# Kernel tuning notes

Hardware: AMD Instinct MI355X
Metric: run time of the kernel (lower is better)

Reference implementation:

```python
import jax, jax.numpy as jnp
import numpy as np
import math

B, N, E = 32, 512, 8192          # graphs, nodes/graph, edges/graph
IN_DIM, D, H, HD, L, C = 64, 128, 4, 32, 3, 10
HID = 2 * D                      # _FeatureMLP hidden = max(d, 2*d)


def _ln(x, g, b, eps=1e-5):
    mu = x.mean(-1, keepdims=True)
    var = ((x - mu) ** 2).mean(-1, keepdims=True)
    return (x - mu) / jnp.sqrt(var + eps) * g + b


def _gelu(x):
    return jax.nn.gelu(x, approximate=False)  # torch nn.GELU default (erf)


def setup_inputs() -> dict:
    key = jax.random.key(0)
    ks = iter(jax.random.split(key, 48))
    def w(*shape):
        return jax.random.normal(next(ks), shape, jnp.float32) * 0.02
    z = lambda *s: jnp.zeros(s, jnp.float32)
    o = lambda *s: jnp.ones(s, jnp.float32)
    return {
        'x': jax.random.normal(next(ks), (B * N, IN_DIM), jnp.float32),
        'src': jax.random.randint(next(ks), (B, E), 0, N),
        'dst': jax.random.randint(next(ks), (B, E), 0, N),
        # node encoder: Linear -> LN -> GELU -> Linear -> LN
        'enc_w1': w(IN_DIM, HID), 'enc_b1': z(HID), 'enc_g1': o(HID), 'enc_bn1': z(HID),
        'enc_w2': w(HID, D), 'enc_b2': z(D), 'enc_g2': o(D), 'enc_bn2': z(D),
        # per-layer edge-message MLP (stacked over L)
        'msg_w1': w(L, 2 * D, D), 'msg_b1': z(L, D),
        'msg_w2': w(L, D, D), 'msg_b2': z(L, D),
        'msg_g': o(L, D), 'msg_bb': z(L, D),
        # per-layer attention
        'qw': w(L, D, H * HD), 'qb': z(L, H * HD),
        'kw': w(L, D, H * HD), 'kb': z(L, H * HD),
        'vw': w(L, D, H * HD), 'vb': z(L, H * HD),
        'ow': w(L, H * HD, D), 'ob': z(L, D),
        'attn_g': o(L, D), 'attn_b': z(L, D),
        # graph head: Linear(4d,2d) -> GELU -> LN -> Linear(2d,C)
        'gh_w1': w(4 * D, 2 * D), 'gh_b1': z(2 * D),
        'gh_g': o(2 * D), 'gh_bn': z(2 * D),
        'gh_w2': w(2 * D, C), 'gh_b2': z(C),
    }


def reference(x, src, dst, enc_w1, enc_b1, enc_g1, enc_bn1, enc_w2, enc_b2, enc_g2, enc_bn2,
              msg_w1, msg_b1, msg_w2, msg_b2, msg_g, msg_bb,
              qw, qb, kw, kb, vw, vb, ow, ob, attn_g, attn_b,
              gh_w1, gh_b1, gh_g, gh_bn, gh_w2, gh_b2):
    # node encoder
    t = _ln(x @ enc_w1 + enc_b1, enc_g1, enc_bn1)
    h = _ln(_gelu(t) @ enc_w2 + enc_b2, enc_g2, enc_bn2)
    h = h.reshape(B, N, D)
    seg = jax.vmap(lambda m, d: jax.ops.segment_sum(m, d, num_segments=N))
    for l in range(L):
        # edge message block: gather src/dst, MLP, scatter-add to dst
        hs = jnp.take_along_axis(h, src[..., None], axis=1)   # [B,E,D]
        hd = jnp.take_along_axis(h, dst[..., None], axis=1)   # [B,E,D]
        m = _gelu(jnp.concatenate([hs, hd], -1) @ msg_w1[l] + msg_b1[l]) @ msg_w2[l] + msg_b2[l]
        h = _ln(h + seg(m, dst), msg_g[l], msg_bb[l])
        # masked attention block (dense per-graph attention)
        q = (h @ qw[l] + qb[l]).reshape(B, N, H, HD)
        k = (h @ kw[l] + kb[l]).reshape(B, N, H, HD)
        v = (h @ vw[l] + vb[l]).reshape(B, N, H, HD)
        scores = jnp.einsum('bnhd,bmhd->bhnm', q, k) / math.sqrt(HD)
        attn = jax.nn.softmax(scores, axis=-1)
        o = jnp.einsum('bhnm,bmhd->bnhd', attn, v).reshape(B, N, H * HD)
        h = _ln(h + o @ ow[l] + ob[l], attn_g[l], attn_b[l])
    # graph pooling: mean | sum | max | std
    mean = h.mean(1)
    summ = h.sum(1)
    mx = h.max(1)
    std = jnp.sqrt(jax.nn.relu((h ** 2).mean(1) - mean ** 2) + 1e-6)
    pool = jnp.concatenate([mean, summ, mx, std], -1)         # [B,4D]
    g = _ln(_gelu(pool @ gh_w1 + gh_b1), gh_g, gh_bn)
    return g @ gh_w2 + gh_b2                                   # [B,C]
```

## Files before the change

kernel.cpp:

```cpp
#include <hip/hip_runtime.h>
#include <cmath>

#define B_   32
#define N_   512
#define E_   8192
#define BN_  16384
#define D_   128

typedef short bf16x8 __attribute__((ext_vector_type(8)));
typedef float f32x4  __attribute__((ext_vector_type(4)));

static __device__ __forceinline__ float bf2f(unsigned short u){
  union{unsigned int i; float f;} v; v.i = ((unsigned int)u)<<16; return v.f;
}
static __device__ __forceinline__ unsigned short f2bf(float f){
  union{unsigned int i; float f;} v; v.f=f;
  unsigned int x=v.i;
  return (unsigned short)((x + 0x7fffu + ((x>>16)&1u))>>16);
}
static __device__ __forceinline__ unsigned int pack2(float a, float b){
  return (unsigned int)f2bf(a) | ((unsigned int)f2bf(b)<<16);
}
static __device__ __forceinline__ float gelu_f(float x){
  float xs=x*0.70710678118654752f;
  float ax=fabsf(xs);
  float t=__builtin_amdgcn_rcpf(1.0f+0.3275911f*ax);
  float p=t*(0.254829592f+t*(-0.284496736f+t*(1.421413741f+t*(-1.453152027f+t*1.061405429f))));
  float er=1.0f - p*__expf(-ax*ax);
  er = (xs<0.f)? -er : er;
  return 0.5f*x*(1.0f+er);
}
static __device__ __forceinline__ float gelu_t(float x){
  float x2=x*x;
  float y=x*(-1.5957691216f + x2*(-0.0713548162f));
  float e=__expf(y);
  return x*__builtin_amdgcn_rcpf(1.0f+e);
}
static __device__ __forceinline__ float ldin(const void* p, size_t i, int isbf){
  return isbf ? bf2f(((const unsigned short*)p)[i]) : ((const float*)p)[i];
}

static __device__ __forceinline__ void block_sum2(float a, float b, float&A, float&Bv, float* red, int nw){
  int lane=threadIdx.x&63, w=threadIdx.x>>6;
  #pragma unroll
  for(int o=32;o>0;o>>=1){ a+=__shfl_down(a,o); b+=__shfl_down(b,o); }
  if(lane==0){ red[w]=a; red[8+w]=b; }
  __syncthreads();
  float sa=0.f, sb=0.f;
  for(int i=0;i<nw;i++){ sa+=red[i]; sb+=red[8+i]; }
  __syncthreads();
  A=sa; Bv=sb;
}

__global__ void sniff_kernel(const unsigned int* __restrict__ xw, int* __restrict__ flag){
  int t=threadIdx.x;
  int cnt=0;
  for(int i=0;i<32;i++){
    unsigned int w=xw[t+64*i];
    float v=bf2f((unsigned short)(w&0xffffu));
    float av=fabsf(v);
    if(v==0.0f || (av>=6e-5f && av<=8.0f)) cnt++;
  }
  #pragma unroll
  for(int o=32;o>0;o>>=1) cnt+=__shfl_down(cnt,o);
  if(t==0) *flag=(cnt>=1024)?1:0;
}

__global__ __launch_bounds__(256) void count_kernel(
  const int* __restrict__ dst, int* __restrict__ cnt)
{
  __shared__ int lc[512];
  int g=blockIdx.x, c=blockIdx.y, t=threadIdx.x;
  for(int i=t;i<512;i+=256) lc[i]=0;
  __syncthreads();
  for(int e=t;e<1024;e+=256) atomicAdd(&lc[dst[(size_t)g*E_+c*1024+e]],1);
  __syncthreads();
  for(int i=t;i<512;i+=256){ int v=lc[i]; if(v) atomicAdd(&cnt[g*512+i],v); }
}

__global__ __launch_bounds__(256) void scan_kernel(
  int* __restrict__ cnt, int* __restrict__ rowptr)
{
  __shared__ int sc[512];
  int g=blockIdx.x, t=threadIdx.x;
  for(int i=t;i<512;i+=256) sc[i]=cnt[g*512+i];
  __syncthreads();
  if(t==0){
    int acc=0;
    for(int i=0;i<512;i++){ int c=sc[i]; rowptr[g*513+i]=acc; cnt[g*512+i]=acc; acc+=c; }
    rowptr[g*513+512]=acc;
  }
}

__global__ __launch_bounds__(256) void scatter_kernel(
  const int* __restrict__ src, const int* __restrict__ dst,
  int* __restrict__ off, unsigned short* __restrict__ ss)
{
  int g=blockIdx.x, c=blockIdx.y, t=threadIdx.x;
  for(int e=t;e<1024;e+=256){
    size_t idx=(size_t)g*E_+c*1024+e;
    int d=dst[idx];
    int pos=atomicAdd(&off[g*512+d],1);
    ss[(size_t)g*E_+pos]=(unsigned short)src[idx];
  }
}

__global__ __launch_bounds__(256) void prep_kernel(
  const void* __restrict__ msg_w1, const void* __restrict__ msg_w2,
  const void* __restrict__ qw, const void* __restrict__ kw,
  const void* __restrict__ vw, const void* __restrict__ ow,
  const void* __restrict__ qb, const void* __restrict__ kb, const void* __restrict__ vb,
  const void* __restrict__ ob, const void* __restrict__ msg_b1, const void* __restrict__ msg_b2,
  const void* __restrict__ msg_g, const void* __restrict__ msg_bb,
  const void* __restrict__ attn_g, const void* __restrict__ attn_b,
  const void* __restrict__ enc_w1, const void* __restrict__ enc_w2,
  const void* __restrict__ enc_b1, const void* __restrict__ enc_g1, const void* __restrict__ enc_bn1,
  const void* __restrict__ enc_b2, const void* __restrict__ enc_g2, const void* __restrict__ enc_bn2,
  const void* __restrict__ gh_w1, const void* __restrict__ gh_w2,
  const void* __restrict__ gh_b1, const void* __restrict__ gh_g,
  const void* __restrict__ gh_bn, const void* __restrict__ gh_b2,
  unsigned short* __restrict__ w1t, unsigned short* __restrict__ w2k,
  unsigned short* __restrict__ qkvt, unsigned short* __restrict__ owt,
  unsigned short* __restrict__ w1te, unsigned short* __restrict__ w2te,
  unsigned short* __restrict__ ghw1t, unsigned short* __restrict__ ghw2t,
  unsigned short* __restrict__ cb, const int* __restrict__ flag)
{
  int isbf=*flag;
  int job=blockIdx.y;
  int i=blockIdx.x*256+threadIdx.x;
  if(job<3){
    if(i<32768){ int l=job; int k=i>>7, n=i&127; w1t[l*32768 + n*256 + k]=f2bf(ldin(msg_w1,(size_t)l*32768+i,isbf)); }
  } else if(job<6){
    int l=job-3; if(i<16384){ w2k[l*16384 + i]=f2bf(ldin(msg_w2,(size_t)l*16384+i,isbf)); }
  } else if(job<15){
    int r=job-6, l=r/3, which=r%3;
    if(i<16384){ int k=i>>7, n=i&127;
      const void* w=(which==0)?qw:((which==1)?kw:vw);
      qkvt[l*49152 + (which*128+n)*128 + k]=f2bf(ldin(w,(size_t)l*16384+i,isbf)); }
  } else if(job<18){
    int l=job-15; if(i<16384){ int k=i>>7, n=i&127; owt[l*16384 + n*128 + k]=f2bf(ldin(ow,(size_t)l*16384+i,isbf)); }
  } else if(job==18){
    if(i<3840){
      float v;
      if(i<1152){ int l=i/384, j=i%384, which=j>>7, jj=j&127;
        const void* bb=(which==0)?qb:((which==1)?kb:vb);
        v=ldin(bb,(size_t)l*128+jj,isbf);
      } else {
        int i2=i-1152; int r=i2/384; int rem=i2%384;
        const void* s = (r==0)?ob:((r==1)?msg_b1:((r==2)?msg_b2:((r==3)?msg_g:((r==4)?msg_bb:((r==5)?attn_g:attn_b)))));
        v=ldin(s,(size_t)rem,isbf);
      }
      cb[i]=f2bf(v);
    }
  } else if(job==19){
    if(i<1152){
      float v;
      if(i<256)       v=ldin(enc_b1,i,isbf);
      else if(i<512)  v=ldin(enc_g1,i-256,isbf);
      else if(i<768)  v=ldin(enc_bn1,i-512,isbf);
      else if(i<896)  v=ldin(enc_b2,i-768,isbf);
      else if(i<1024) v=ldin(enc_g2,i-896,isbf);
      else            v=ldin(enc_bn2,i-1024,isbf);
      cb[3840+i]=f2bf(v);
    }
  } else if(job==20){
    if(i<16384){ int k=i>>8, n=i&255; w1te[n*64+k]=f2bf(ldin(enc_w1,(size_t)i,isbf)); }
  } else if(job==21){
    if(i<32768){ int k=i>>7, n=i&127; w2te[n*256+k]=f2bf(ldin(enc_w2,(size_t)i,isbf)); }
  } else if(job<26){
    int p=job-22; int j=p*32768+i;
    if(i<32768){ int k=j>>8, n=j&255; ghw1t[n*512+k]=f2bf(ldin(gh_w1,(size_t)j,isbf)); }
  } else {
    if(i<2560){ int k=i/10, n=i%10; ghw2t[n*256+k]=f2bf(ldin(gh_w2,(size_t)i,isbf)); }
    else if(i<2560+778){
      int j=i-2560; float v;
      if(j<256)      v=ldin(gh_b1,j,isbf);
      else if(j<512) v=ldin(gh_g,j-256,isbf);
      else if(j<768) v=ldin(gh_bn,j-512,isbf);
      else           v=ldin(gh_b2,j-768,isbf);
      cb[4992+j]=f2bf(v);
    }
  }
}

__global__ __launch_bounds__(256) void enc_kernel(
  const void* __restrict__ x, const unsigned short* __restrict__ w1te,
  const unsigned short* __restrict__ w2te, const unsigned short* __restrict__ cb,
  unsigned short* __restrict__ h, const int* __restrict__ flag)
{
  __shared__ __align__(16) unsigned short xs[64][72];
  __shared__ __align__(16) unsigned short t1[64][264];
  int isbf=*flag;
  int m0=blockIdx.x*64;
  int t=threadIdx.x, lane=t&63, w=t>>6, quad=lane>>4, ln=lane&15;
  for(int c2=t;c2<1024;c2+=256){
    int i=c2*4, row=i>>6, col=i&63;
    float v0,v1,v2,v3;
    if(isbf){
      const unsigned short* p=(const unsigned short*)x+(size_t)m0*64+i;
      v0=bf2f(p[0]); v1=bf2f(p[1]); v2=bf2f(p[2]); v3=bf2f(p[3]);
    } else {
      float4 f=*(const float4*)((const float*)x+(size_t)m0*64+i);
      v0=f.x; v1=f.y; v2=f.z; v3=f.w;
    }
    ushort4 o; o.x=f2bf(v0); o.y=f2bf(v1); o.z=f2bf(v2); o.w=f2bf(v3);
    *(ushort4*)&xs[row][col]=o;
  }
  __syncthreads();
  f32x4 a[4][4];
  #pragma unroll
  for(int nt=0;nt<4;nt++){ a[nt][0]={0,0,0,0}; a[nt][1]={0,0,0,0}; a[nt][2]={0,0,0,0}; a[nt][3]={0,0,0,0}; }
  #pragma unroll
  for(int k0i=0;k0i<2;k0i++){
    bf16x8 af[4];
    #pragma unroll
    for(int f=0;f<4;f++) af[f]=*(const bf16x8*)(&xs[f*16+ln][k0i*32+quad*8]);
    #pragma unroll
    for(int nt=0;nt<4;nt++){
      int n=w*64+nt*16+ln;
      bf16x8 bfr=*(const bf16x8*)(w1te+(size_t)n*64+k0i*32+quad*8);
      #pragma unroll
      for(int f=0;f<4;f++) a[nt][f]=__builtin_amdgcn_mfma_f32_16x16x32_bf16(af[f],bfr,a[nt][f],0,0,0);
    }
  }
  #pragma unroll
  for(int nt=0;nt<4;nt++){
    int n=w*64+nt*16+ln;
    float bv=bf2f(cb[3840+n]);
    #pragma unroll
    for(int f=0;f<4;f++)
      #pragma unroll
      for(int r=0;r<4;r++) t1[f*16+quad*4+r][n]=f2bf(a[nt][f][r]+bv);
  }
  __syncthreads();
  {
    int row=t>>2, qq=t&3;
    float s=0.f,s2=0.f;
    for(int c=qq*64;c<qq*64+64;c++){ float v=bf2f(t1[row][c]); s+=v; s2+=v*v; }
    s+=__shfl_xor(s,1); s+=__shfl_xor(s,2);
    s2+=__shfl_xor(s2,1); s2+=__shfl_xor(s2,2);
    float mu=s*(1.f/256.f), var=fmaxf(s2*(1.f/256.f)-mu*mu,0.f);
    float rr=rsqrtf(var+1e-5f);
    for(int c=qq*64;c<qq*64+64;c++){
      float v=bf2f(t1[row][c]);
      t1[row][c]=f2bf(gelu_f((v-mu)*rr*bf2f(cb[4096+c])+bf2f(cb[4352+c])));
    }
  }
  __syncthreads();
  f32x4 b2a[2][4];
  #pragma unroll
  for(int nt=0;nt<2;nt++){ b2a[nt][0]={0,0,0,0}; b2a[nt][1]={0,0,0,0}; b2a[nt][2]={0,0,0,0}; b2a[nt][3]={0,0,0,0}; }
  #pragma unroll
  for(int k0i=0;k0i<8;k0i++){
    bf16x8 af[4];
    #pragma unroll
    for(int f=0;f<4;f++) af[f]=*(const bf16x8*)(&t1[f*16+ln][k0i*32+quad*8]);
    #pragma unroll
    for(int nt=0;nt<2;nt++){
      int n=w*32+nt*16+ln;
      bf16x8 bfr=*(const bf16x8*)(w2te+(size_t)n*256+k0i*32+quad*8);
      #pragma unroll
      for(int f=0;f<4;f++) b2a[nt][f]=__builtin_amdgcn_mfma_f32_16x16x32_bf16(af[f],bfr,b2a[nt][f],0,0,0);
    }
  }
  __syncthreads();
  float* mf=(float*)&t1[0][0];
  #pragma unroll
  for(int nt=0;nt<2;nt++){
    int n=w*32+nt*16+ln;
    float bv=bf2f(cb[4608+n]);
    #pragma unroll
    for(int f=0;f<4;f++)
      #pragma unroll
      for(int r=0;r<4;r++) mf[(f*16+quad*4+r)*132+n]=b2a[nt][f][r]+bv;
  }
  __syncthreads();
  {
    int row=t>>2, qq=t&3;
    float s=0.f,s2=0.f;
    for(int c=qq*32;c<qq*32+32;c++){ float v=mf[row*132+c]; s+=v; s2+=v*v; }
    s+=__shfl_xor(s,1); s+=__shfl_xor(s,2);
    s2+=__shfl_xor(s2,1); s2+=__shfl_xor(s2,2);
    float mu=s*(1.f/128.f), var=fmaxf(s2*(1.f/128.f)-mu*mu,0.f);
    float rr=rsqrtf(var+1e-5f);
    for(int c=qq*32;c<qq*32+32;c+=2){
      float v0=(mf[row*132+c  ]-mu)*rr*bf2f(cb[4736+c  ])+bf2f(cb[4864+c  ]);
      float v1=(mf[row*132+c+1]-mu)*rr*bf2f(cb[4736+c+1])+bf2f(cb[4864+c+1]);
      *(unsigned int*)(h+(size_t)(m0+row)*128+c)=pack2(v0,v1);
    }
  }
}

__global__ __launch_bounds__(256) void uvgen_kernel(
  const unsigned short* __restrict__ hrows, const unsigned short* __restrict__ w1t,
  const unsigned short* __restrict__ b1, unsigned short* __restrict__ UV)
{
  __shared__ __align__(16) unsigned short a_t[64][136];
  int t=threadIdx.x;
  int m0=blockIdx.x*64;
  int y=blockIdx.y;
  for(int c=t;c<1024;c+=256){
    int m=c>>4, pp=c&15;
    *(uint4*)&a_t[m][pp*8]=*((const uint4*)(hrows+(size_t)(m0+m)*128)+pp);
  }
  __syncthreads();
  int lane=t&63, w=t>>6, quad=lane>>4, ln=lane&15;
  #pragma unroll
  for(int nt=0;nt<2;nt++){
    int n=w*32+nt*16+ln;
    f32x4 a0={0,0,0,0},a1={0,0,0,0},a2={0,0,0,0},a3={0,0,0,0};
    const unsigned short* wp=w1t+(size_t)n*256+y*128+quad*8;
    #pragma unroll
    for(int k0=0;k0<128;k0+=32){
      bf16x8 bfr=*(const bf16x8*)(wp+k0);
      bf16x8 f0=*(const bf16x8*)(&a_t[ln   ][k0+quad*8]);
      bf16x8 f1=*(const bf16x8*)(&a_t[16+ln][k0+quad*8]);
      bf16x8 f2=*(const bf16x8*)(&a_t[32+ln][k0+quad*8]);
      bf16x8 f3=*(const bf16x8*)(&a_t[48+ln][k0+quad*8]);
      a0=__builtin_amdgcn_mfma_f32_16x16x32_bf16(f0,bfr,a0,0,0,0);
      a1=__builtin_amdgcn_mfma_f32_16x16x32_bf16(f1,bfr,a1,0,0,0);
      a2=__builtin_amdgcn_mfma_f32_16x16x32_bf16(f2,bfr,a2,0,0,0);
      a3=__builtin_amdgcn_mfma_f32_16x16x32_bf16(f3,bfr,a3,0,0,0);
    }
    float bv=y?0.f:bf2f(b1[n]);
    #pragma unroll
    for(int r2=0;r2<4;r2++){
      UV[(size_t)(m0+quad*4+r2   )*256+y*128+n]=f2bf(a0[r2]+bv);
      UV[(size_t)(m0+16+quad*4+r2)*256+y*128+n]=f2bf(a1[r2]+bv);
      UV[(size_t)(m0+32+quad*4+r2)*256+y*128+n]=f2bf(a2[r2]+bv);
      UV[(size_t)(m0+48+quad*4+r2)*256+y*128+n]=f2bf(a3[r2]+bv);
    }
  }
}

__global__ __launch_bounds__(256) void qkvgen_kernel(
  const unsigned short* __restrict__ hrows, const unsigned short* __restrict__ wqkv,
  const unsigned short* __restrict__ bqkv,
  unsigned short* __restrict__ Qb, unsigned short* __restrict__ Kb,
  unsigned short* __restrict__ Vtb)
{
  __shared__ __align__(16) unsigned short a_t[64][136];
  int t=threadIdx.x;
  int m0=blockIdx.x*64;
  int y=blockIdx.y;
  for(int c=t;c<1024;c+=256){
    int m=c>>4, pp=c&15;
    *(uint4*)&a_t[m][pp*8]=*((const uint4*)(hrows+(size_t)(m0+m)*128)+pp);
  }
  __syncthreads();
  int lane=t&63, w=t>>6, quad=lane>>4, ln=lane&15;
  int gloc=m0>>9, r0=m0&511;
  #pragma unroll
  for(int nt=0;nt<2;nt++){
    int n=w*32+nt*16+ln;
    f32x4 a0={0,0,0,0},a1={0,0,0,0},a2={0,0,0,0},a3={0,0,0,0};
    const unsigned short* wp=wqkv+(size_t)(y*128+n)*128+quad*8;
    #pragma unroll
    for(int k0=0;k0<128;k0+=32){
      bf16x8 bfr=*(const bf16x8*)(wp+k0);
      bf16x8 f0=*(const bf16x8*)(&a_t[ln   ][k0+quad*8]);
      bf16x8 f1=*(const bf16x8*)(&a_t[16+ln][k0+quad*8]);
      bf16x8 f2=*(const bf16x8*)(&a_t[32+ln][k0+quad*8]);
      bf16x8 f3=*(const bf16x8*)(&a_t[48+ln][k0+quad*8]);
      a0=__builtin_amdgcn_mfma_f32_16x16x32_bf16(f0,bfr,a0,0,0,0);
      a1=__builtin_amdgcn_mfma_f32_16x16x32_bf16(f1,bfr,a1,0,0,0);
      a2=__builtin_amdgcn_mfma_f32_16x16x32_bf16(f2,bfr,a2,0,0,0);
      a3=__builtin_amdgcn_mfma_f32_16x16x32_bf16(f3,bfr,a3,0,0,0);
    }
    float bv=bf2f(bqkv[y*128+n]);
    if(y==0){
      const float sc=0.17677669529663689f;
      #pragma unroll
      for(int r=0;r<4;r++){
        Qb[(size_t)(m0   +quad*4+r)*128+n]=f2bf((a0[r]+bv)*sc);
        Qb[(size_t)(m0+16+quad*4+r)*128+n]=f2bf((a1[r]+bv)*sc);
        Qb[(size_t)(m0+32+quad*4+r)*128+n]=f2bf((a2[r]+bv)*sc);
        Qb[(size_t)(m0+48+quad*4+r)*128+n]=f2bf((a3[r]+bv)*sc);
      }
    } else if(y==1){
      #pragma unroll
      for(int r=0;r<4;r++){
        Kb[(size_t)(m0   +quad*4+r)*128+n]=f2bf(a0[r]+bv);
        Kb[(size_t)(m0+16+quad*4+r)*128+n]=f2bf(a1[r]+bv);
        Kb[(size_t)(m0+32+quad*4+r)*128+n]=f2bf(a2[r]+bv);
        Kb[(size_t)(m0+48+quad*4+r)*128+n]=f2bf(a3[r]+bv);
      }
    } else {
      unsigned short* vrow = Vtb + ((size_t)gloc*128+n)*512 + r0 + quad*4;
      ushort4 o;
      o.x=f2bf(a0[0]+bv); o.y=f2bf(a0[1]+bv); o.z=f2bf(a0[2]+bv); o.w=f2bf(a0[3]+bv);
      *(ushort4*)(vrow)=o;
      o.x=f2bf(a1[0]+bv); o.y=f2bf(a1[1]+bv); o.z=f2bf(a1[2]+bv); o.w=f2bf(a1[3]+bv);
      *(ushort4*)(vrow+16)=o;
      o.x=f2bf(a2[0]+bv); o.y=f2bf(a2[1]+bv); o.z=f2bf(a2[2]+bv); o.w=f2bf(a2[3]+bv);
      *(ushort4*)(vrow+32)=o;
      o.x=f2bf(a3[0]+bv); o.y=f2bf(a3[1]+bv); o.z=f2bf(a3[2]+bv); o.w=f2bf(a3[3]+bv);
      *(ushort4*)(vrow+48)=o;
    }
  }
}

__global__ __launch_bounds__(128) void edgef_kernel(
  unsigned short* __restrict__ h,
  const unsigned short* __restrict__ UV,
  const unsigned short* __restrict__ ss,
  const int* __restrict__ rowptr,
  const unsigned short* __restrict__ w2k,
  const unsigned short* __restrict__ b2,
  const unsigned short* __restrict__ gg, const unsigned short* __restrict__ bbp,
  int b0, int gEp)
{
  __shared__ __align__(16) float aggL[2][4][128];
  __shared__ __align__(16) float po[2][4][128];
  int t=threadIdx.x, lane=t&63, w=t>>6;
  int bid=blockIdx.x;
  int lg=bid%gEp, ch=bid/gEp;
  int g=b0+lg;
  const unsigned short* UVg = UV + (size_t)lg*512*256;
  const unsigned short* ssg = ss + (size_t)g*E_;
  int dbase = ch*4;
  int bnd[5];
  #pragma unroll
  for(int i=0;i<5;i++) bnd[i]=rowptr[g*513+dbase+i];
  #pragma unroll 1
  for(int dd=0;dd<4;dd++){
    int e_lo=bnd[dd], e_hi0=bnd[dd+1];
    int half=(e_hi0-e_lo+1)>>1;
    int es = w ? (e_lo+half) : e_lo;
    int ee = w ? e_hi0       : (e_lo+half);
    unsigned int vdw=*(const unsigned int*)(UVg + (size_t)(dbase+dd)*256 + 128 + lane*2);
    float v0=bf2f((unsigned short)(vdw&0xffffu)), v1=bf2f((unsigned short)(vdw>>16));
    float a0=0.f, a1=0.f;
    int si3,si4,si5;
    unsigned int u0,u1,u2;
    {
      int s0=__builtin_amdgcn_readfirstlane((int)ssg[es  ])&511;
      int s1=__builtin_amdgcn_readfirstlane((int)ssg[es+1])&511;
      int s2=__builtin_amdgcn_readfirstlane((int)ssg[es+2])&511;
      si3=(int)ssg[es+3]; si4=(int)ssg[es+4]; si5=(int)ssg[es+5];
      u0=*(const unsigned int*)(UVg + (size_t)s0*256 + lane*2);
      u1=*(const unsigned int*)(UVg + (size_t)s1*256 + lane*2);
      u2=*(const unsigned int*)(UVg + (size_t)s2*256 + lane*2);
    }
    #pragma unroll 2
    for(int e=es;e<ee;e++){
      float z0=bf2f((unsigned short)(u0&0xffffu))+v0;
      float z1=bf2f((unsigned short)(u0>>16))+v1;
      u0=u1; u1=u2;
      int s3=__builtin_amdgcn_readfirstlane(si3)&511;
      u2=*(const unsigned int*)(UVg + (size_t)s3*256 + lane*2);
      si3=si4; si4=si5;
      si5=(int)ssg[e+6];
      a0+=gelu_t(z0); a1+=gelu_t(z1);
    }
    aggL[w][dd][lane*2  ]=a0;
    aggL[w][dd][lane*2+1]=a1;
  }
  __syncthreads();
  float o[4][2];
  #pragma unroll
  for(int dd=0;dd<4;dd++){ o[dd][0]=0.f; o[dd][1]=0.f; }
  #pragma unroll 4
  for(int kk=0;kk<64;kk++){
    int k=w*64+kk;
    unsigned int wdw=*(const unsigned int*)(w2k+(size_t)k*128+lane*2);
    float w0=bf2f((unsigned short)(wdw&0xffffu));
    float w1=bf2f((unsigned short)(wdw>>16));
    #pragma unroll
    for(int dd=0;dd<4;dd++){
      float av=aggL[0][dd][k]+aggL[1][dd][k];
      o[dd][0]+=av*w0; o[dd][1]+=av*w1;
    }
  }
  #pragma unroll
  for(int dd=0;dd<4;dd++){
    po[w][dd][lane*2  ]=o[dd][0];
    po[w][dd][lane*2+1]=o[dd][1];
  }
  __syncthreads();
  #pragma unroll 1
  for(int p=0;p<2;p++){
    int di=w*2+p;
    int d = dbase + di;
    float deg=(float)(bnd[di+1]-bnd[di]);
    float o0=bf2f(b2[lane*2  ])*deg + po[0][di][lane*2  ] + po[1][di][lane*2  ];
    float o1=bf2f(b2[lane*2+1])*deg + po[0][di][lane*2+1] + po[1][di][lane*2+1];
    size_t base=(size_t)(g*512+d)*128;
    unsigned int hdw=*(const unsigned int*)(h+base+lane*2);
    float x0=bf2f((unsigned short)(hdw&0xffffu))+o0;
    float x1=bf2f((unsigned short)(hdw>>16))+o1;
    float s1=x0+x1, s2=x0*x0+x1*x1;
    #pragma unroll
    for(int off=32;off>0;off>>=1){ s1+=__shfl_xor(s1,off); s2+=__shfl_xor(s2,off); }
    float mu=s1*(1.f/128.f), var=fmaxf(s2*(1.f/128.f)-mu*mu,0.f);
    float rr=rsqrtf(var+1e-5f);
    float y0=(x0-mu)*rr*bf2f(gg[lane*2  ])+bf2f(bbp[lane*2  ]);
    float y1=(x1-mu)*rr*bf2f(gg[lane*2+1])+bf2f(bbp[lane*2+1]);
    *(unsigned int*)(h+base+lane*2)=pack2(y0,y1);
  }
}

__global__ __launch_bounds__(256) void attnf_kernel(
  const unsigned short* __restrict__ Qb, const unsigned short* __restrict__ Kb,
  const unsigned short* __restrict__ Vtb, unsigned short* __restrict__ obuf, int gA)
{
  __shared__ __align__(16) unsigned short Ps[64][72];
  int bx=blockIdx.x;
  int lg=bx%gA; int rr2=bx/gA; int hh=rr2&3, qq4=rr2>>2;
  int t=threadIdx.x, lane=t&63, w=t>>6, quad=lane>>4, ln=lane&15;
  const unsigned short* Kg = Kb + (size_t)lg*65536 + hh*32;
  const unsigned short* Vg = Vtb + ((size_t)lg*128+hh*32)*512;
  bf16x8 qf[2];
  #pragma unroll
  for(int qt=0;qt<2;qt++)
    qf[qt]=*(const bf16x8*)(Qb + (size_t)(lg*512+qq4*128+qt*64+w*16+ln)*128 + hh*32 + quad*8);
  f32x4 O[2][2]; float Lp[2][4];
  #pragma unroll
  for(int qt=0;qt<2;qt++){ O[qt][0]={0,0,0,0}; O[qt][1]={0,0,0,0};
    #pragma unroll
    for(int r=0;r<4;r++) Lp[qt][r]=0.f; }
  for(int kc=0;kc<8;kc++){
    bf16x8 kf[4];
    #pragma unroll
    for(int f=0;f<4;f++) kf[f]=*(const bf16x8*)(Kg + (size_t)(kc*64+f*16+ln)*128 + quad*8);
    bf16x8 va[2], vb[2];
    #pragma unroll
    for(int s2=0;s2<2;s2++){
      va[s2]=*(const bf16x8*)(Vg + (size_t)ln*512      + kc*64 + s2*32 + quad*8);
      vb[s2]=*(const bf16x8*)(Vg + (size_t)(16+ln)*512 + kc*64 + s2*32 + quad*8);
    }
    #pragma unroll
    for(int qt=0;qt<2;qt++){
      f32x4 s[4];
      #pragma unroll
      for(int f=0;f<4;f++){
        f32x4 z={0,0,0,0};
        s[f]=__builtin_amdgcn_mfma_f32_16x16x32_bf16(qf[qt],kf[f],z,0,0,0);
      }
      #pragma unroll
      for(int f=0;f<4;f++)
        #pragma unroll
        for(int r=0;r<4;r++){
          float pe=__expf(fminf(s[f][r],30.0f));
          Ps[w*16+quad*4+r][f*16+ln]=f2bf(pe);
          Lp[qt][r]+=pe;
        }
      #pragma unroll
      for(int s2=0;s2<2;s2++){
        bf16x8 pf=*(const bf16x8*)(&Ps[w*16+ln][s2*32+quad*8]);
        O[qt][0]=__builtin_amdgcn_mfma_f32_16x16x32_bf16(pf,va[s2],O[qt][0],0,0,0);
        O[qt][1]=__builtin_amdgcn_mfma_f32_16x16x32_bf16(pf,vb[s2],O[qt][1],0,0,0);
      }
    }
  }
  #pragma unroll
  for(int qt=0;qt<2;qt++){
    #pragma unroll
    for(int o=1;o<16;o<<=1)
      #pragma unroll
      for(int r=0;r<4;r++) Lp[qt][r]+=__shfl_xor(Lp[qt][r],o);
    #pragma unroll
    for(int r=0;r<4;r++){
      float inv=1.0f/Lp[qt][r];
      size_t row=(size_t)lg*512+qq4*128+qt*64+w*16+quad*4+r;
      obuf[row*128+hh*32+ln   ]=f2bf(O[qt][0][r]*inv);
      obuf[row*128+hh*32+16+ln]=f2bf(O[qt][1][r]*inv);
    }
  }
}

__global__ __launch_bounds__(256) void oproj_kernel(
  const unsigned short* __restrict__ obuf, const unsigned short* __restrict__ wo,
  const unsigned short* __restrict__ bo, unsigned short* __restrict__ h,
  const unsigned short* __restrict__ gg, const unsigned short* __restrict__ bbp, int b0)
{
  __shared__ __align__(16) unsigned short a_t[64][136];
  __shared__ float mf[64][132];
  int t=threadIdx.x, lane=t&63, w=t>>6, quad=lane>>4, ln=lane&15;
  int m0=blockIdx.x*64;
  for(int c=t;c<64*16;c+=256){
    int m=c>>4, pp=c&15;
    *(uint4*)&a_t[m][pp*8]=*((const uint4*)(obuf+(size_t)(m0+m)*128)+pp);
  }
  __syncthreads();
  #pragma unroll
  for(int nt=0;nt<2;nt++){
    int n=w*32+nt*16+ln;
    f32x4 a0={0,0,0,0},a1={0,0,0,0},a2={0,0,0,0},a3={0,0,0,0};
    const unsigned short* wp=wo+(size_t)n*128+quad*8;
    #pragma unroll
    for(int k0=0;k0<128;k0+=32){
      bf16x8 bfr=*(const bf16x8*)(wp+k0);
      bf16x8 f0=*(const bf16x8*)(&a_t[ln   ][k0+quad*8]);
      bf16x8 f1=*(const bf16x8*)(&a_t[16+ln][k0+quad*8]);
      bf16x8 f2=*(const bf16x8*)(&a_t[32+ln][k0+quad*8]);
      bf16x8 f3=*(const bf16x8*)(&a_t[48+ln][k0+quad*8]);
      a0=__builtin_amdgcn_mfma_f32_16x16x32_bf16(f0,bfr,a0,0,0,0);
      a1=__builtin_amdgcn_mfma_f32_16x16x32_bf16(f1,bfr,a1,0,0,0);
      a2=__builtin_amdgcn_mfma_f32_16x16x32_bf16(f2,bfr,a2,0,0,0);
      a3=__builtin_amdgcn_mfma_f32_16x16x32_bf16(f3,bfr,a3,0,0,0);
    }
    float bv=bf2f(bo[n]);
    #pragma unroll
    for(int r=0;r<4;r++){
      mf[quad*4+r   ][n]=a0[r]+bv;
      mf[16+quad*4+r][n]=a1[r]+bv;
      mf[32+quad*4+r][n]=a2[r]+bv;
      mf[48+quad*4+r][n]=a3[r]+bv;
    }
  }
  __syncthreads();
  {
    int row=t>>2, qq=t&3;
    size_t base=(size_t)(b0*512+m0+row)*128;
    float s=0.f,s2=0.f;
    float vals[32];
    for(int j=0;j<32;j++){
      int c=qq*32+j;
      float v=bf2f(h[base+c])+mf[row][c];
      vals[j]=v; s+=v; s2+=v*v;
    }
    s+=__shfl_xor(s,1); s+=__shfl_xor(s,2);
    s2+=__shfl_xor(s2,1); s2+=__shfl_xor(s2,2);
    float mu=s*(1.f/128.f), var=fmaxf(s2*(1.f/128.f)-mu*mu,0.f);
    float rr=rsqrtf(var+1e-5f);
    for(int j=0;j<32;j+=2){
      int c=qq*32+j;
      float v0=(vals[j]  -mu)*rr*bf2f(gg[c  ])+bf2f(bbp[c  ]);
      float v1=(vals[j+1]-mu)*rr*bf2f(gg[c+1])+bf2f(bbp[c+1]);
      *(unsigned int*)(h+base+c)=pack2(v0,v1);
    }
  }
}

__global__ __launch_bounds__(256) void poolp_kernel(
  const unsigned short* __restrict__ h, float* __restrict__ part)
{
  __shared__ float ps[256], ps2[256], pm[256];
  int b=blockIdx.x, c=blockIdx.y;
  int t=threadIdx.x, d=t&127, hf=t>>7;
  float s=0.f,s2=0.f,mx=-1e30f;
  for(int r=hf*32;r<hf*32+32;r++){
    float v=bf2f(h[((size_t)(b*512+c*64+r))*128+d]);
    s+=v; s2+=v*v; mx=fmaxf(mx,v);
  }
  ps[t]=s; ps2[t]=s2; pm[t]=mx;
  __syncthreads();
  if(t<128){
    s=ps[t]+ps[128+t]; s2=ps2[t]+ps2[128+t]; mx=fmaxf(pm[t],pm[128+t]);
    size_t base=((size_t)(b*8+c))*384;
    part[base+t]=s; part[base+128+t]=s2; part[base+256+t]=mx;
  }
}

__global__ __launch_bounds__(256) void head_kernel(
  const float* __restrict__ part, const unsigned short* __restrict__ ghw1t,
  const unsigned short* __restrict__ ghw2t, const unsigned short* __restrict__ cb,
  void* __restrict__ out, const int* __restrict__ flag)
{
  int isbf=*flag;
  int b=blockIdx.x, t=threadIdx.x;
  __shared__ float pl[512];
  __shared__ float gl[256];
  __shared__ float red[16];
  if(t<128){
    float s=0.f,s2=0.f,mx=-1e30f;
    for(int c=0;c<8;c++){
      size_t base=((size_t)(b*8+c))*384;
      s += part[base+t];
      s2+= part[base+128+t];
      mx = fmaxf(mx, part[base+256+t]);
    }
    float mean=s*(1.f/512.f);
    float var=fmaxf(s2*(1.f/512.f)-mean*mean,0.f);
    float sd=sqrtf(var+1e-6f);
    pl[t]=mean; pl[128+t]=s; pl[256+t]=mx; pl[384+t]=sd;
  }
  __syncthreads();
  float a=bf2f(cb[4992+t]);
  const unsigned short* wr=ghw1t+(size_t)t*512;
  for(int k0=0;k0<512;k0+=8){
    bf16x8 wv=*(const bf16x8*)(wr+k0);
    const unsigned short* wp=(const unsigned short*)&wv;
    #pragma unroll
    for(int j=0;j<8;j++) a+=pl[k0+j]*bf2f(wp[j]);
  }
  float u=gelu_f(a);
  float S,S2; block_sum2(u,u*u,S,S2,red,4);
  float mu=S*(1.f/256.f), var=fmaxf(S2*(1.f/256.f)-mu*mu,0.f);
  float r=rsqrtf(var+1e-5f);
  gl[t]=(u-mu)*r*bf2f(cb[5248+t])+bf2f(cb[5504+t]);
  __syncthreads();
  if(t<10){
    float o=bf2f(cb[5760+t]);
    const unsigned short* wr2=ghw2t+(size_t)t*256;
    for(int k0=0;k0<256;k0+=8){
      bf16x8 wv=*(const bf16x8*)(wr2+k0);
      const unsigned short* wp=(const unsigned short*)&wv;
      #pragma unroll
      for(int j=0;j<8;j++) o+=gl[k0+j]*bf2f(wp[j]);
    }
    if(isbf) ((unsigned short*)out)[b*10+t]=f2bf(o);
    else     ((float*)out)[b*10+t]=o;
  }
}

extern "C" void kernel_launch(void* const* d_in, const int* in_sizes, int n_in,
                              void* d_out, int out_size, void* d_ws, size_t ws_size,
                              hipStream_t stream)
{
  const void* x      =d_in[0];
  const int*  src    =(const int*)d_in[1];
  const int*  dstp   =(const int*)d_in[2];
  const void* enc_w1 =d_in[3];  const void* enc_b1 =d_in[4];
  const void* enc_g1 =d_in[5];  const void* enc_bn1=d_in[6];
  const void* enc_w2 =d_in[7];  const void* enc_b2 =d_in[8];
  const void* enc_g2 =d_in[9];  const void* enc_bn2=d_in[10];
  const void* msg_w1 =d_in[11]; const void* msg_b1 =d_in[12];
  const void* msg_w2 =d_in[13]; const void* msg_b2 =d_in[14];
  const void* msg_g  =d_in[15]; const void* msg_bb =d_in[16];
  const void* qw     =d_in[17]; const void* qb     =d_in[18];
  const void* kw     =d_in[19]; const void* kb     =d_in[20];
  const void* vw     =d_in[21]; const void* vb     =d_in[22];
  const void* ow     =d_in[23]; const void* ob     =d_in[24];
  const void* attn_g =d_in[25]; const void* attn_b =d_in[26];
  const void* gh_w1  =d_in[27]; const void* gh_b1  =d_in[28];
  const void* gh_g   =d_in[29]; const void* gh_bn  =d_in[30];
  const void* gh_w2  =d_in[31]; const void* gh_b2  =d_in[32];
  (void)in_sizes; (void)n_in; (void)out_size;

  char* base=(char*)d_ws;
  unsigned short* h    =(unsigned short*)(base);
  unsigned short* w1t  =(unsigned short*)(base + 4194304);
  unsigned short* w2k  =(unsigned short*)(base + 4390912);
  unsigned short* qkvt =(unsigned short*)(base + 4489216);
  unsigned short* owt  =(unsigned short*)(base + 4784128);
  unsigned short* w1te =(unsigned short*)(base + 4882432);
  unsigned short* w2te =(unsigned short*)(base + 4915200);
  unsigned short* ghw1t=(unsigned short*)(base + 4980736);
  unsigned short* ghw2t=(unsigned short*)(base + 5242880);
  unsigned short* cb   =(unsigned short*)(base + 5248000);
  int*   rowptr        =(int*)(base + 5325312);
  int*   flag          =(int*)(base + 5390976);
  int*   cnt           =(int*)(base + 5391360);
  unsigned short* ssrt =(unsigned short*)(base + 5505024);
  char* R              = base + 6029312;

  size_t Rcap = (ws_size > 6029312) ? (ws_size - 6029312) : 0;
  int gA = 32;  while(gA  > 4 && (size_t)gA *524288 > Rcap) gA  >>= 1;
  int gEp= 32;  while(gEp > 4 && (size_t)gEp*262144 > Rcap) gEp >>= 1;
  int epass = 32/gEp, apass = 32/gA;
  float* part=(float*)R;

  sniff_kernel<<<1,64,0,stream>>>((const unsigned int*)x, flag);
  hipMemsetAsync(cnt,0,65536,stream);
  count_kernel<<<dim3(B_,8),256,0,stream>>>(dstp,cnt);
  scan_kernel<<<B_,256,0,stream>>>(cnt,rowptr);
  scatter_kernel<<<dim3(B_,8),256,0,stream>>>(src,dstp,cnt,ssrt);
  prep_kernel<<<dim3(128,27),256,0,stream>>>(msg_w1,msg_w2,qw,kw,vw,ow,qb,kb,vb,
      ob,msg_b1,msg_b2,msg_g,msg_bb,attn_g,attn_b,
      enc_w1,enc_w2,enc_b1,enc_g1,enc_bn1,enc_b2,enc_g2,enc_bn2,
      gh_w1,gh_w2,gh_b1,gh_g,gh_bn,gh_b2,
      w1t,w2k,qkvt,owt,w1te,w2te,ghw1t,ghw2t,cb,flag);

  enc_kernel<<<BN_/64,256,0,stream>>>(x,w1te,w2te,cb,h,flag);

  for(int l=0;l<3;l++){
    for(int ep=0;ep<epass;ep++){
      int b0=ep*gEp;
      unsigned short* UV=(unsigned short*)R;
      uvgen_kernel<<<dim3(gEp*8,2),256,0,stream>>>(h+(size_t)b0*512*128,
          w1t+(size_t)l*32768, cb+1536+l*128, UV);
      edgef_kernel<<<gEp*128,128,0,stream>>>(h,UV,ssrt,rowptr,
          w2k+(size_t)l*16384, cb+1920+l*128, cb+2304+l*128, cb+2688+l*128, b0, gEp);
    }
    for(int ap=0;ap<apass;ap++){
      int b0=ap*gA;
      unsigned short* Qb  =(unsigned short*)R;
      unsigned short* Kb  =Qb  + (size_t)gA*65536;
      unsigned short* Vtb =Kb  + (size_t)gA*65536;
      unsigned short* obuf=Vtb + (size_t)gA*65536;
      qkvgen_kernel<<<dim3(gA*8,3),256,0,stream>>>(h+(size_t)b0*512*128,
          qkvt+(size_t)l*49152, cb+l*384, Qb, Kb, Vtb);
      attnf_kernel<<<gA*16,256,0,stream>>>(Qb, Kb, Vtb, obuf, gA);
      oproj_kernel<<<gA*8,256,0,stream>>>(obuf, owt+(size_t)l*16384,
          cb+1152+l*128, h, cb+3072+l*128, cb+3456+l*128, b0);
    }
  }
  poolp_kernel<<<dim3(B_,8),256,0,stream>>>(h,part);
  head_kernel<<<B_,256,0,stream>>>(part,ghw1t,ghw2t,cb,d_out,flag);
}
```

Baseline: 426.8 us.

## Fuse UV generation into encoder/attention epilogues and merge attention with output projection

Removes the standalone uvgen and oproj kernels. The edge-message U/V projection now runs in the epilogue of the encoder (layer 0) and of the attention kernel (next layer). Attention is restructured so each block handles 32 query rows across all 4 heads, which lets it do the output projection and LayerNorm locally and skip the obuf round-trip through global memory. UV is now a full-batch buffer, so the edge kernel launches once per layer, at the cost of more workspace and larger, register-heavier fused kernels.

Result: faster. 387.9 us (-9.1%).

```diff
diff --git a/kernel.cpp b/kernel.cpp
--- a/kernel.cpp
+++ b/kernel.cpp
@@ -186,7 +186,8 @@
 __global__ __launch_bounds__(256) void enc_kernel(
   const void* __restrict__ x, const unsigned short* __restrict__ w1te,
   const unsigned short* __restrict__ w2te, const unsigned short* __restrict__ cb,
-  unsigned short* __restrict__ h, const int* __restrict__ flag)
+  unsigned short* __restrict__ h, const int* __restrict__ flag,
+  const unsigned short* __restrict__ w1t0, unsigned short* __restrict__ UV)
 {
   __shared__ __align__(16) unsigned short xs[64][72];
   __shared__ __align__(16) unsigned short t1[64][264];
@@ -277,58 +278,54 @@
   __syncthreads();
   {
     int row=t>>2, qq=t&3;
+    float vals[32];
     float s=0.f,s2=0.f;
-    for(int c=qq*32;c<qq*32+32;c++){ float v=mf[row*132+c]; s+=v; s2+=v*v; }
+    for(int j=0;j<32;j++){ float v=mf[row*132+qq*32+j]; vals[j]=v; s+=v; s2+=v*v; }
     s+=__shfl_xor(s,1); s+=__shfl_xor(s,2);
     s2+=__shfl_xor(s2,1); s2+=__shfl_xor(s2,2);
     float mu=s*(1.f/128.f), var=fmaxf(s2*(1.f/128.f)-mu*mu,0.f);
     float rr=rsqrtf(var+1e-5f);
-    for(int c=qq*32;c<qq*32+32;c+=2){
-      float v0=(mf[row*132+c  ]-mu)*rr*bf2f(cb[4736+c  ])+bf2f(cb[4864+c  ]);
-      float v1=(mf[row*132+c+1]-mu)*rr*bf2f(cb[4736+c+1])+bf2f(cb[4864+c+1]);
+    for(int j=0;j<32;j+=2){
+      int c=qq*32+j;
+      float v0=(vals[j]  -mu)*rr*bf2f(cb[4736+c  ])+bf2f(cb[4864+c  ]);
+      float v1=(vals[j+1]-mu)*rr*bf2f(cb[4736+c+1])+bf2f(cb[4864+c+1]);
       *(unsigned int*)(h+(size_t)(m0+row)*128+c)=pack2(v0,v1);
-    }
-  }
-}
-
-__global__ __launch_bounds__(256) void uvgen_kernel(
-  const unsigned short* __restrict__ hrows, const unsigned short* __restrict__ w1t,
-  const unsigned short* __restrict__ b1, unsigned short* __restrict__ UV)
-{
-  __shared__ __align__(16) unsigned short a_t[64][136];
-  int t=threadIdx.x;
-  int m0=blockIdx.x*64;
-  int y=blockIdx.y;
-  for(int c=t;c<1024;c+=256){
-    int m=c>>4, pp=c&15;
-    *(uint4*)&a_t[m][pp*8]=*((const uint4*)(hrows+(size_t)(m0+m)*128)+pp);
-  }
-  __syncthreads();
-  int lane=t&63, w=t>>6, quad=lane>>4, ln=lane&15;
-  #pragma unroll
-  for(int nt=0;nt<2;nt++){
-    int n=w*32+nt*16+ln;
-    f32x4 a0={0,0,0,0},a1={0,0,0,0},a2={0,0,0,0},a3={0,0,0,0};
-    const unsigned short* wp=w1t+(size_t)n*256+y*128+quad*8;
-    #pragma unroll
-    for(int k0=0;k0<128;k0+=32){
-      bf16x8 bfr=*(const bf16x8*)(wp+k0);
-      bf16x8 f0=*(const bf16x8*)(&a_t[ln   ][k0+quad*8]);
-      bf16x8 f1=*(const bf16x8*)(&a_t[16+ln][k0+quad*8]);
-      bf16x8 f2=*(const bf16x8*)(&a_t[32+ln][k0+quad*8]);
-      bf16x8 f3=*(const bf16x8*)(&a_t[48+ln][k0+quad*8]);
-      a0=__builtin_amdgcn_mfma_f32_16x16x32_bf16(f0,bfr,a0,0,0,0);
-      a1=__builtin_amdgcn_mfma_f32_16x16x32_bf16(f1,bfr,a1,0,0,0);
-      a2=__builtin_amdgcn_mfma_f32_16x16x32_bf16(f2,bfr,a2,0,0,0);
-      a3=__builtin_amdgcn_mfma_f32_16x16x32_bf16(f3,bfr,a3,0,0,0);
-    }
-    float bv=y?0.f:bf2f(b1[n]);
-    #pragma unroll
-    for(int r2=0;r2<4;r2++){
-      UV[(size_t)(m0+quad*4+r2   )*256+y*128+n]=f2bf(a0[r2]+bv);
-      UV[(size_t)(m0+16+quad*4+r2)*256+y*128+n]=f2bf(a1[r2]+bv);
-      UV[(size_t)(m0+32+quad*4+r2)*256+y*128+n]=f2bf(a2[r2]+bv);
-      UV[(size_t)(m0+48+quad*4+r2)*256+y*128+n]=f2bf(a3[r2]+bv);
+      vals[j]=v0; vals[j+1]=v1;
+    }
+    __syncthreads();
+    unsigned short* hb=&t1[0][0];
+    for(int j=0;j<32;j++) hb[row*136+qq*32+j]=f2bf(vals[j]);
+  }
+  __syncthreads();
+  {
+    const unsigned short* hb=&t1[0][0];
+    #pragma unroll
+    for(int y=0;y<2;y++)
+    #pragma unroll
+    for(int nt=0;nt<2;nt++){
+      int n=w*32+nt*16+ln;
+      f32x4 a0={0,0,0,0},a1={0,0,0,0},a2={0,0,0,0},a3={0,0,0,0};
+      const unsigned short* wp=w1t0+(size_t)n*256+y*128+quad*8;
+      #pragma unroll
+      for(int k0=0;k0<128;k0+=32){
+        bf16x8 bfr=*(const bf16x8*)(wp+k0);
+        bf16x8 f0=*(const bf16x8*)(hb+(size_t)(ln   )*136+k0+quad*8);
+        bf16x8 f1=*(const bf16x8*)(hb+(size_t)(16+ln)*136+k0+quad*8);
+        bf16x8 f2=*(const bf16x8*)(hb+(size_t)(32+ln)*136+k0+quad*8);
+        bf16x8 f3=*(const bf16x8*)(hb+(size_t)(48+ln)*136+k0+quad*8);
+        a0=__builtin_amdgcn_mfma_f32_16x16x32_bf16(f0,bfr,a0,0,0,0);
+        a1=__builtin_amdgcn_mfma_f32_16x16x32_bf16(f1,bfr,a1,0,0,0);
+        a2=__builtin_amdgcn_mfma_f32_16x16x32_bf16(f2,bfr,a2,0,0,0);
+        a3=__builtin_amdgcn_mfma_f32_16x16x32_bf16(f3,bfr,a3,0,0,0);
+      }
+      float bv=y?0.f:bf2f(cb[1536+n]);
+      #pragma unroll
+      for(int r=0;r<4;r++){
+        UV[(size_t)(m0   +quad*4+r)*256+y*128+n]=f2bf(a0[r]+bv);
+        UV[(size_t)(m0+16+quad*4+r)*256+y*128+n]=f2bf(a1[r]+bv);
+        UV[(size_t)(m0+32+quad*4+r)*256+y*128+n]=f2bf(a2[r]+bv);
+        UV[(size_t)(m0+48+quad*4+r)*256+y*128+n]=f2bf(a3[r]+bv);
+      }
     }
   }
 }
@@ -416,7 +413,7 @@
   int bid=blockIdx.x;
   int lg=bid%gEp, ch=bid/gEp;
   int g=b0+lg;
-  const unsigned short* UVg = UV + (size_t)lg*512*256;
+  const unsigned short* UVg = UV + (size_t)g*512*256;
   const unsigned short* ssg = ss + (size_t)g*E_;
   int dbase = ch*4;
   int bnd[5];
@@ -500,20 +497,30 @@
   }
 }
 
-__global__ __launch_bounds__(256) void attnf_kernel(
+__global__ __launch_bounds__(256) void attn_fused_kernel(
   const unsigned short* __restrict__ Qb, const unsigned short* __restrict__ Kb,
-  const unsigned short* __restrict__ Vtb, unsigned short* __restrict__ obuf, int gA)
-{
-  __shared__ __align__(16) unsigned short Ps[64][72];
+  const unsigned short* __restrict__ Vtb,
+  const unsigned short* __restrict__ wo, const unsigned short* __restrict__ bo,
+  unsigned short* __restrict__ h,
+  const unsigned short* __restrict__ gg, const unsigned short* __restrict__ bbp,
+  const unsigned short* __restrict__ w1tn, const unsigned short* __restrict__ b1n,
+  unsigned short* __restrict__ UV, int b0, int gA, int do_uv)
+{
+  __shared__ __align__(16) unsigned short hO[32][136];
+  __shared__ __align__(16) unsigned short Psh[4][16][72];
+  __shared__ __align__(16) float mf[32][132];
   int bx=blockIdx.x;
-  int lg=bx%gA; int rr2=bx/gA; int hh=rr2&3, qq4=rr2>>2;
+  int lg=bx%gA, ch=bx/gA;
+  int r0=ch*32;
+  int g=b0+lg;
   int t=threadIdx.x, lane=t&63, w=t>>6, quad=lane>>4, ln=lane&15;
-  const unsigned short* Kg = Kb + (size_t)lg*65536 + hh*32;
-  const unsigned short* Vg = Vtb + ((size_t)lg*128+hh*32)*512;
+  const unsigned short* Qg = Qb + (size_t)lg*65536;
+  const unsigned short* Kg = Kb + (size_t)lg*65536 + w*32;
+  const unsigned short* Vg = Vtb + ((size_t)lg*128 + w*32)*512;
   bf16x8 qf[2];
   #pragma unroll
   for(int qt=0;qt<2;qt++)
-    qf[qt]=*(const bf16x8*)(Qb + (size_t)(lg*512+qq4*128+qt*64+w*16+ln)*128 + hh*32 + quad*8);
+    qf[qt]=*(const bf16x8*)(Qg + (size_t)(r0+qt*16+ln)*128 + w*32 + quad*8);
   f32x4 O[2][2]; float Lp[2][4];
   #pragma unroll
   for(int qt=0;qt<2;qt++){ O[qt][0]={0,0,0,0}; O[qt][1]={0,0,0,0};
@@ -542,12 +549,12 @@
         #pragma unroll
         for(int r=0;r<4;r++){
           float pe=__expf(fminf(s[f][r],30.0f));
-          Ps[w*16+quad*4+r][f*16+ln]=f2bf(pe);
+          Psh[w][quad*4+r][f*16+ln]=f2bf(pe);
           Lp[qt][r]+=pe;
         }
       #pragma unroll
       for(int s2=0;s2<2;s2++){
-        bf16x8 pf=*(const bf16x8*)(&Ps[w*16+ln][s2*32+quad*8]);
+        bf16x8 pf=*(const bf16x8*)(&Psh[w][ln][s2*32+quad*8]);
         O[qt][0]=__builtin_amdgcn_mfma_f32_16x16x32_bf16(pf,va[s2],O[qt][0],0,0,0);
         O[qt][1]=__builtin_amdgcn_mfma_f32_16x16x32_bf16(pf,vb[s2],O[qt][1],0,0,0);
       }
@@ -562,73 +569,78 @@
     #pragma unroll
     for(int r=0;r<4;r++){
       float inv=1.0f/Lp[qt][r];
-      size_t row=(size_t)lg*512+qq4*128+qt*64+w*16+quad*4+r;
-      obuf[row*128+hh*32+ln   ]=f2bf(O[qt][0][r]*inv);
-      obuf[row*128+hh*32+16+ln]=f2bf(O[qt][1][r]*inv);
-    }
-  }
-}
-
-__global__ __launch_bounds__(256) void oproj_kernel(
-  const unsigned short* __restrict__ obuf, const unsigned short* __restrict__ wo,
-  const unsigned short* __restrict__ bo, unsigned short* __restrict__ h,
-  const unsigned short* __restrict__ gg, const unsigned short* __restrict__ bbp, int b0)
-{
-  __shared__ __align__(16) unsigned short a_t[64][136];
-  __shared__ float mf[64][132];
-  int t=threadIdx.x, lane=t&63, w=t>>6, quad=lane>>4, ln=lane&15;
-  int m0=blockIdx.x*64;
-  for(int c=t;c<64*16;c+=256){
-    int m=c>>4, pp=c&15;
-    *(uint4*)&a_t[m][pp*8]=*((const uint4*)(obuf+(size_t)(m0+m)*128)+pp);
+      int qr=qt*16+quad*4+r;
+      hO[qr][w*32+ln   ]=f2bf(O[qt][0][r]*inv);
+      hO[qr][w*32+16+ln]=f2bf(O[qt][1][r]*inv);
+    }
   }
   __syncthreads();
   #pragma unroll
   for(int nt=0;nt<2;nt++){
     int n=w*32+nt*16+ln;
-    f32x4 a0={0,0,0,0},a1={0,0,0,0},a2={0,0,0,0},a3={0,0,0,0};
+    f32x4 a0={0,0,0,0},a1={0,0,0,0};
     const unsigned short* wp=wo+(size_t)n*128+quad*8;
     #pragma unroll
     for(int k0=0;k0<128;k0+=32){
       bf16x8 bfr=*(const bf16x8*)(wp+k0);
-      bf16x8 f0=*(const bf16x8*)(&a_t[ln   ][k0+quad*8]);
-      bf16x8 f1=*(const bf16x8*)(&a_t[16+ln][k0+quad*8]);
-      bf16x8 f2=*(const bf16x8*)(&a_t[32+ln][k0+quad*8]);
-      bf16x8 f3=*(const bf16x8*)(&a_t[48+ln][k0+quad*8]);
+      bf16x8 f0=*(const bf16x8*)(&hO[ln   ][k0+quad*8]);
+      bf16x8 f1=*(const bf16x8*)(&hO[16+ln][k0+quad*8]);
       a0=__builtin_amdgcn_mfma_f32_16x16x32_bf16(f0,bfr,a0,0,0,0);
       a1=__builtin_amdgcn_mfma_f32_16x16x32_bf16(f1,bfr,a1,0,0,0);
-      a2=__builtin_amdgcn_mfma_f32_16x16x32_bf16(f2,bfr,a2,0,0,0);
-      a3=__builtin_amdgcn_mfma_f32_16x16x32_bf16(f3,bfr,a3,0,0,0);
     }
     float bv=bf2f(bo[n]);
     #pragma unroll
     for(int r=0;r<4;r++){
       mf[quad*4+r   ][n]=a0[r]+bv;
       mf[16+quad*4+r][n]=a1[r]+bv;
-      mf[32+quad*4+r][n]=a2[r]+bv;
-      mf[48+quad*4+r][n]=a3[r]+bv;
     }
   }
   __syncthreads();
   {
-    int row=t>>2, qq=t&3;
-    size_t base=(size_t)(b0*512+m0+row)*128;
+    int row=t>>3, oct=t&7;
+    size_t base=((size_t)(g*512+r0+row))*128;
+    float vals[16];
     float s=0.f,s2=0.f;
-    float vals[32];
-    for(int j=0;j<32;j++){
-      int c=qq*32+j;
+    for(int j=0;j<16;j++){
+      int c=oct*16+j;
       float v=bf2f(h[base+c])+mf[row][c];
       vals[j]=v; s+=v; s2+=v*v;
     }
-    s+=__shfl_xor(s,1); s+=__shfl_xor(s,2);
-    s2+=__shfl_xor(s2,1); s2+=__shfl_xor(s2,2);
+    s+=__shfl_xor(s,1); s+=__shfl_xor(s,2); s+=__shfl_xor(s,4);
+    s2+=__shfl_xor(s2,1); s2+=__shfl_xor(s2,2); s2+=__shfl_xor(s2,4);
     float mu=s*(1.f/128.f), var=fmaxf(s2*(1.f/128.f)-mu*mu,0.f);
     float rr=rsqrtf(var+1e-5f);
-    for(int j=0;j<32;j+=2){
-      int c=qq*32+j;
-      float v0=(vals[j]  -mu)*rr*bf2f(gg[c  ])+bf2f(bbp[c  ]);
-      float v1=(vals[j+1]-mu)*rr*bf2f(gg[c+1])+bf2f(bbp[c+1]);
-      *(unsigned int*)(h+base+c)=pack2(v0,v1);
+    for(int j=0;j<16;j+=2){
+      int c=oct*16+j;
+      float y0=(vals[j]  -mu)*rr*bf2f(gg[c  ])+bf2f(bbp[c  ]);
+      float y1=(vals[j+1]-mu)*rr*bf2f(gg[c+1])+bf2f(bbp[c+1]);
+      *(unsigned int*)(h+base+c)=pack2(y0,y1);
+      hO[row][c]=f2bf(y0); hO[row][c+1]=f2bf(y1);
+    }
+  }
+  if(!do_uv) return;
+  __syncthreads();
+  #pragma unroll
+  for(int y=0;y<2;y++)
+  #pragma unroll
+  for(int nt=0;nt<2;nt++){
+    int n=w*32+nt*16+ln;
+    f32x4 a0={0,0,0,0},a1={0,0,0,0};
+    const unsigned short* wp=w1tn+(size_t)n*256+y*128+quad*8;
+    #pragma unroll
+    for(int k0=0;k0<128;k0+=32){
+      bf16x8 bfr=*(const bf16x8*)(wp+k0);
+      bf16x8 f0=*(const bf16x8*)(&hO[ln   ][k0+quad*8]);
+      bf16x8 f1=*(const bf16x8*)(&hO[16+ln][k0+quad*8]);
+      a0=__builtin_amdgcn_mfma_f32_16x16x32_bf16(f0,bfr,a0,0,0,0);
+      a1=__builtin_amdgcn_mfma_f32_16x16x32_bf16(f1,bfr,a1,0,0,0);
+    }
+    float bv=y?0.f:bf2f(b1n[n]);
+    size_t rb=(size_t)(g*512+r0);
+    #pragma unroll
+    for(int r=0;r<4;r++){
+      UV[(rb   +quad*4+r)*256+y*128+n]=f2bf(a0[r]+bv);
+      UV[(rb+16+quad*4+r)*256+y*128+n]=f2bf(a1[r]+bv);
     }
   }
 }
@@ -747,9 +759,13 @@
   char* R              = base + 6029312;
 
   size_t Rcap = (ws_size > 6029312) ? (ws_size - 6029312) : 0;
-  int gA = 32;  while(gA  > 4 && (size_t)gA *524288 > Rcap) gA  >>= 1;
-  int gEp= 32;  while(gEp > 4 && (size_t)gEp*262144 > Rcap) gEp >>= 1;
-  int epass = 32/gEp, apass = 32/gA;
+  int gA = 32;
+  while(gA > 4 && 8388608 + (size_t)gA*393216 > Rcap) gA >>= 1;
+  int apass = 32/gA;
+  unsigned short* UV  =(unsigned short*)R;
+  unsigned short* Qb  =UV  + 4194304;
+  unsigned short* Kb  =Qb  + (size_t)gA*65536;
+  unsigned short* Vtb =Kb  + (size_t)gA*65536;
   float* part=(float*)R;
 
   sniff_kernel<<<1,64,0,stream>>>((const unsigned int*)x, flag);
@@ -763,28 +779,19 @@
       gh_w1,gh_w2,gh_b1,gh_g,gh_bn,gh_b2,
       w1t,w2k,qkvt,owt,w1te,w2te,ghw1t,ghw2t,cb,flag);
 
-  enc_kernel<<<BN_/64,256,0,stream>>>(x,w1te,w2te,cb,h,flag);
+  enc_kernel<<<BN_/64,256,0,stream>>>(x,w1te,w2te,cb,h,flag,w1t,UV);
 
   for(int l=0;l<3;l++){
-    for(int ep=0;ep<epass;ep++){
-      int b0=ep*gEp;
-      unsigned short* UV=(unsigned short*)R;
-      uvgen_kernel<<<dim3(gEp*8,2),256,0,stream>>>(h+(size_t)b0*512*128,
-          w1t+(size_t)l*32768, cb+1536+l*128, UV);
-      edgef_kernel<<<gEp*128,128,0,stream>>>(h,UV,ssrt,rowptr,
-          w2k+(size_t)l*16384, cb+1920+l*128, cb+2304+l*128, cb+2688+l*128, b0, gEp);
-    }
+    edgef_kernel<<<32*128,128,0,stream>>>(h,UV,ssrt,rowptr,
+        w2k+(size_t)l*16384, cb+1920+l*128, cb+2304+l*128, cb+2688+l*128, 0, 32);
+    int ln=(l+1)%3;
     for(int ap=0;ap<apass;ap++){
       int b0=ap*gA;
-      unsigned short* Qb  =(unsigned short*)R;
-      unsigned short* Kb  =Qb  + (size_t)gA*65536;
-      unsigned short* Vtb =Kb  + (size_t)gA*65536;
-      unsigned short* obuf=Vtb + (size_t)gA*65536;
       qkvgen_kernel<<<dim3(gA*8,3),256,0,stream>>>(h+(size_t)b0*512*128,
           qkvt+(size_t)l*49152, cb+l*384, Qb, Kb, Vtb);
-      attnf_kernel<<<gA*16,256,0,stream>>>(Qb, Kb, Vtb, obuf, gA);
-      oproj_kernel<<<gA*8,256,0,stream>>>(obuf, owt+(size_t)l*16384,
-          cb+1152+l*128, h, cb+3072+l*128, cb+3456+l*128, b0);
+      attn_fused_kernel<<<gA*16,256,0,stream>>>(Qb, Kb, Vtb,
+          owt+(size_t)l*16384, cb+1152+l*128, h, cb+3072+l*128, cb+3456+l*128,
+          w1t+(size_t)ln*32768, cb+1536+ln*128, UV, b0, gA, (l<2)?1:0);
     }
   }
   poolp_kernel<<<dim3(B_,8),256,0,stream>>>(h,part);
```
